# Kernel optimization log

Hardware: AMD Instinct MI355X
Metric: run time of the kernel (lower is better)

Reference implementation:

```python
import math
import jax, jax.numpy as jnp
import numpy as np

NEG_INF_FILL = 1e-09  # faithful to the source: masked positions get +1e-09, not -inf

B, H, S, D = 2, 16, 2048, 64


def setup_inputs() -> dict:
    key = jax.random.key(0)
    kq, kk, kv = jax.random.split(key, 3)
    q = jax.random.normal(kq, (B, H, S, D), dtype=jnp.float32)
    k = jax.random.normal(kk, (B, H, S, D), dtype=jnp.float32)
    v = jax.random.normal(kv, (B, H, S, D), dtype=jnp.float32)
    # causal boolean mask, broadcast over heads: [B, 1, S, S]
    causal = jnp.tril(jnp.ones((S, S), dtype=bool))
    attention_mask = jnp.broadcast_to(causal[None, None, :, :], (B, 1, S, S))
    return {"q": q, "k": k, "v": v, "attention_mask": attention_mask}


def reference(q, k, v, attention_mask):
    d_k = q.shape[-1]
    # scores: [B, H, S, S]
    scores = jnp.einsum("bhqd,bhkd->bhqk", q, k) / math.sqrt(d_k)
    scores = jnp.where(attention_mask, scores, NEG_INF_FILL)
    attn = jax.nn.softmax(scores, axis=-1)
    # output: [B, H, S, D]
    return jnp.einsum("bhqk,bhkd->bhqd", attn, v)
```

## Files before the change

kernel.cpp:

```cpp
#include <hip/hip_runtime.h>


#define SEQ 2048
#define DIM 64
#define NKT 32
#define KS_STRIDE 72
#define PS_STRIDE 72
#define QSCALE 0.18033688011112042f

typedef _Float16 half_t;
typedef _Float16 half8  __attribute__((ext_vector_type(8)));
typedef _Float16 half4v __attribute__((ext_vector_type(4)));
typedef _Float16 half2v __attribute__((ext_vector_type(2)));
typedef float    float4v __attribute__((ext_vector_type(4)));

#define KIMG_HALFS ((size_t)4194304)
#define WS_NEED    ((size_t)16777216)

__global__ __launch_bounds__(256)
void prep_kernel(const float* __restrict__ K, const float* __restrict__ V,
                 half_t* __restrict__ Kimg, half_t* __restrict__ VTimg) {
    __shared__ __align__(16) half_t vt[64 * 72];
    const int kt = blockIdx.x, bh = blockIdx.y;
    const int tid = threadIdx.x;
    const float* Kt = K + ((size_t)bh * SEQ + kt * 64) * DIM;
    const float* Vt = V + ((size_t)bh * SEQ + kt * 64) * DIM;
    half_t* Kd = Kimg  + (((size_t)(bh * NKT + kt)) << 12);
    half_t* Vd = VTimg + (((size_t)(bh * NKT + kt)) << 12);

    {
        const int row = tid >> 2, q = tid & 3;
        const float* src = Kt + row * DIM + 16 * q;
        #pragma unroll
        for (int cc = 0; cc < 2; ++cc) {
            float4v a = *(const float4v*)(src + 8 * cc);
            float4v b = *(const float4v*)(src + 8 * cc + 4);
            half8 hh;
            hh[0]=(half_t)a[0]; hh[1]=(half_t)a[1]; hh[2]=(half_t)a[2]; hh[3]=(half_t)a[3];
            hh[4]=(half_t)b[0]; hh[5]=(half_t)b[1]; hh[6]=(half_t)b[2]; hh[7]=(half_t)b[3];
            *(half8*)(Kd + row * 64 + 16 * q + 8 * cc) = hh;
        }
    }
    {
        const int c = tid & 15, r0 = tid >> 4;
        #pragma unroll
        for (int u = 0; u < 2; ++u) {
            const float* vp = Vt + (size_t)(2 * (r0 + 16 * u)) * DIM + 4 * c;
            float4v x0 = *(const float4v*)(vp);
            float4v x1 = *(const float4v*)(vp + DIM);
            #pragma unroll
            for (int i = 0; i < 4; ++i) {
                const int d = 4 * c + i;
                vt[d * 72 + 2 * (r0 + 16 * u)]     = (half_t)x0[i];
                vt[d * 72 + 2 * (r0 + 16 * u) + 1] = (half_t)x1[i];
            }
        }
    }
    __syncthreads();
    {
        const int d = tid >> 2, g = tid & 3;
        #pragma unroll
        for (int cc = 0; cc < 2; ++cc) {
            const int c0 = 2 * g + cc;
            half8 hh = *(const half8*)(vt + d * 72 + 8 * c0);
            *(half8*)(Vd + d * 64 + 8 * c0) = hh;
        }
    }
}

__global__ __launch_bounds__(256, 4)
void attn_mfma_kernel(const float* __restrict__ Q,
                      const half_t* __restrict__ Kimg,
                      const half_t* __restrict__ VTimg,
                      const float* __restrict__ V,
                      float* __restrict__ O) {
    __shared__ __align__(16) half_t smem_h[64 * KS_STRIDE + 64 * KS_STRIDE + 4 * 16 * PS_STRIDE];
    half_t* Ks  = smem_h;
    half_t* VTs = smem_h + 64 * KS_STRIDE;
    half_t* Ps  = smem_h + 2 * 64 * KS_STRIDE;

    const int tid = threadIdx.x;
    const int l   = tid & 63;
    const int w   = tid >> 6;
    const int lx  = l & 15;
    const int h   = l >> 4;
    const int bh  = blockIdx.x;
    const int qb  = 31 - (int)blockIdx.y;
    const int qbase = qb * 64;
    const int nkt = qb + 1;
    const int n_tail = SEQ - nkt * 64;

    const float* Qh = Q + (size_t)bh * SEQ * DIM;
    const float* Vh = V + (size_t)bh * SEQ * DIM;
    float*       Oh = O + (size_t)bh * SEQ * DIM;
    const half_t* Kimg_b = Kimg  + (((size_t)(bh * NKT)) << 12);
    const half_t* Vimg_b = VTimg + (((size_t)(bh * NKT)) << 12);

    half8 qf[2];
    const int qrow_w = qbase + 16 * w;
    {
        const float* qp = Qh + (size_t)(qrow_w + lx) * DIM;
        #pragma unroll
        for (int s = 0; s < 2; ++s) {
            float4v a = *(const float4v*)(qp + 32 * s + 8 * h);
            float4v b = *(const float4v*)(qp + 32 * s + 8 * h + 4);
            half8 f;
            f[0] = (half_t)(a[0] * QSCALE); f[1] = (half_t)(a[1] * QSCALE);
            f[2] = (half_t)(a[2] * QSCALE); f[3] = (half_t)(a[3] * QSCALE);
            f[4] = (half_t)(b[0] * QSCALE); f[5] = (half_t)(b[1] * QSCALE);
            f[6] = (half_t)(b[2] * QSCALE); f[7] = (half_t)(b[3] * QSCALE);
            qf[s] = f;
        }
    }

    float4v acc[4];
    #pragma unroll
    for (int mt = 0; mt < 4; ++mt) acc[mt] = (float4v){0.f, 0.f, 0.f, 0.f};
    float lp = 0.f;

    const int soff = tid << 3;
    const int srow = tid >> 3;
    const int sc8  = (tid & 7) << 3;
    half8 kh0, kh1, vh0, vh1;
    auto load_tile = [&](int kt) {
        const half_t* Kt16 = Kimg_b + ((size_t)kt << 12);
        const half_t* Vt16 = Vimg_b + ((size_t)kt << 12);
        kh0 = *(const half8*)(Kt16 + soff);
        kh1 = *(const half8*)(Kt16 + soff + 2048);
        vh0 = *(const half8*)(Vt16 + soff);
        vh1 = *(const half8*)(Vt16 + soff + 2048);
    };

    load_tile(0);

    for (int kt = 0; kt < nkt; ++kt) {
        __syncthreads();

        *(half8*)(Ks  + srow * KS_STRIDE + sc8)        = kh0;
        *(half8*)(Ks  + (srow + 32) * KS_STRIDE + sc8) = kh1;
        *(half8*)(VTs + srow * KS_STRIDE + sc8)        = vh0;
        *(half8*)(VTs + (srow + 32) * KS_STRIDE + sc8) = vh1;
        __syncthreads();

        if (kt + 1 < nkt) load_tile(kt + 1);

        const int key_base = kt * 64;
        #pragma unroll
        for (int mt = 0; mt < 4; ++mt) {
            half8 ak0 = *(const half8*)(Ks + (16 * mt + lx) * KS_STRIDE + 8 * h);
            half8 ak1 = *(const half8*)(Ks + (16 * mt + lx) * KS_STRIDE + 32 + 8 * h);
            const bool need_mask = (key_base + 16 * mt + 15) > qrow_w;
            float4v ct = (float4v){0.f, 0.f, 0.f, 0.f};
            ct = __builtin_amdgcn_mfma_f32_16x16x32_f16(ak0, qf[0], ct, 0, 0, 0);
            ct = __builtin_amdgcn_mfma_f32_16x16x32_f16(ak1, qf[1], ct, 0, 0, 0);
            float p[4];
            #pragma unroll
            for (int r = 0; r < 4; ++r)
                p[r] = __builtin_amdgcn_exp2f(ct[r]);
            if (need_mask) {
                const int qg = qrow_w + lx;
                const int kb = key_base + 16 * mt + 4 * h;
                #pragma unroll
                for (int r = 0; r < 4; ++r)
                    if (kb + r > qg) p[r] = 1.0f;
            }
            lp += (p[0] + p[1]) + (p[2] + p[3]);
            half4v hp;
            hp[0] = (half_t)p[0]; hp[1] = (half_t)p[1];
            hp[2] = (half_t)p[2]; hp[3] = (half_t)p[3];
            *(half4v*)(Ps + w * (16 * PS_STRIDE) + lx * PS_STRIDE + 16 * mt + 4 * h) = hp;
        }

        half8 pf[2];
        #pragma unroll
        for (int s = 0; s < 2; ++s)
            pf[s] = *(const half8*)(Ps + w * (16 * PS_STRIDE) + lx * PS_STRIDE
                                    + 32 * s + 8 * h);
        #pragma unroll
        for (int mtd = 0; mtd < 4; ++mtd) {
            half8 av0 = *(const half8*)(VTs + (16 * mtd + lx) * KS_STRIDE + 8 * h);
            half8 av1 = *(const half8*)(VTs + (16 * mtd + lx) * KS_STRIDE + 32 + 8 * h);
            float4v ct = acc[mtd];
            ct = __builtin_amdgcn_mfma_f32_16x16x32_f16(av0, pf[0], ct, 0, 0, 0);
            ct = __builtin_amdgcn_mfma_f32_16x16x32_f16(av1, pf[1], ct, 0, 0, 0);
            acc[mtd] = ct;
        }
    }

    float s_l = lp;
    s_l += __shfl_xor(s_l, 16, 64);
    s_l += __shfl_xor(s_l, 32, 64);
    const float linv = 1.0f / (s_l + (float)n_tail);

    float ts0 = 0.f, ts1 = 0.f, ts2 = 0.f, ts3 = 0.f;
    {
        const int c = tid & 15, r0 = tid >> 4;
        const int tstart = nkt * 64;
        #pragma unroll 4
        for (int k = tstart + r0; k < SEQ; k += 16) {
            float4v x = *(const float4v*)(Vh + (size_t)k * DIM + 4 * c);
            ts0 += x[0]; ts1 += x[1]; ts2 += x[2]; ts3 += x[3];
        }
    }
    __syncthreads();
    float* preS = (float*)smem_h;
    float* vtf  = ((float*)smem_h) + 4160;
    {
        const int c = tid & 15, r0 = tid >> 4;
        float4v pv = {ts0, ts1, ts2, ts3};
        *(float4v*)(preS + r0 * 68 + 4 * c) = pv;
    }
    __syncthreads();
    if (tid < 64) {
        float s = 0.f;
        #pragma unroll
        for (int p = 0; p < 16; ++p) s += preS[p * 68 + tid];
        vtf[tid] = s;
    }
    __syncthreads();
    float vt_l[4][4];
    #pragma unroll
    for (int mt = 0; mt < 4; ++mt)
        #pragma unroll
        for (int r = 0; r < 4; ++r) vt_l[mt][r] = vtf[16 * mt + 4 * h + r];

    float* Osm = (float*)smem_h;
    #pragma unroll
    for (int mt = 0; mt < 4; ++mt)
        #pragma unroll
        for (int r = 0; r < 4; ++r) {
            float o = (acc[mt][r] + vt_l[mt][r]) * linv;
            Osm[w * (16 * 65) + lx * 65 + 16 * mt + 4 * h + r] = o;
        }
    __syncthreads();
    {
        const int c = tid & 15, r0 = tid >> 4;
        #pragma unroll
        for (int u = 0; u < 4; ++u) {
            const int row = r0 + 16 * u;
            const int dc = 4 * c;
            const float* src = Osm + (row >> 4) * (16 * 65) + (row & 15) * 65 + dc;
            float4v ov = {src[0], src[1], src[2], src[3]};
            *(float4v*)(Oh + (size_t)(qbase + row) * DIM + dc) = ov;
        }
    }
}

__global__ __launch_bounds__(256, 4)
void attn_mfma_fallback(const float* __restrict__ Q,
                        const float* __restrict__ K,
                        const float* __restrict__ V,
                        float* __restrict__ O) {
    __shared__ half_t smem_h[64 * KS_STRIDE + 64 * KS_STRIDE + 4 * 16 * PS_STRIDE];
    half_t* Ks  = smem_h;
    half_t* VTs = smem_h + 64 * KS_STRIDE;
    half_t* Ps  = smem_h + 2 * 64 * KS_STRIDE;

    const int tid = threadIdx.x;
    const int l   = tid & 63;
    const int w   = tid >> 6;
    const int lx  = l & 15;
    const int h   = l >> 4;
    const int bh  = blockIdx.x;
    const int qb  = 31 - (int)blockIdx.y;
    const int qbase = qb * 64;
    const int nkt = qb + 1;
    const int n_tail = SEQ - nkt * 64;

    const float* Qh = Q + (size_t)bh * SEQ * DIM;
    const float* Kh = K + (size_t)bh * SEQ * DIM;
    const float* Vh = V + (size_t)bh * SEQ * DIM;
    float*       Oh = O + (size_t)bh * SEQ * DIM;

    half8 qf[2];
    const int qrow_w = qbase + 16 * w;
    {
        const float* qp = Qh + (size_t)(qrow_w + lx) * DIM;
        #pragma unroll
        for (int s = 0; s < 2; ++s) {
            float4v a = *(const float4v*)(qp + 32 * s + 8 * h);
            float4v b = *(const float4v*)(qp + 32 * s + 8 * h + 4);
            half8 f;
            f[0] = (half_t)(a[0] * QSCALE); f[1] = (half_t)(a[1] * QSCALE);
            f[2] = (half_t)(a[2] * QSCALE); f[3] = (half_t)(a[3] * QSCALE);
            f[4] = (half_t)(b[0] * QSCALE); f[5] = (half_t)(b[1] * QSCALE);
            f[6] = (half_t)(b[2] * QSCALE); f[7] = (half_t)(b[3] * QSCALE);
            qf[s] = f;
        }
    }

    float4v acc[4];
    #pragma unroll
    for (int mt = 0; mt < 4; ++mt) acc[mt] = (float4v){0.f, 0.f, 0.f, 0.f};
    float lp = 0.f;

    const int c  = tid & 15;
    const int r0 = tid >> 4;

    float4v kreg[4], vreg[4];
    auto load_tile = [&](int kt) {
        const float* Kt = Kh + (size_t)kt * 64 * DIM;
        const float* Vt = Vh + (size_t)kt * 64 * DIM;
        #pragma unroll
        for (int u = 0; u < 4; ++u)
            kreg[u] = *(const float4v*)(Kt + (r0 + 16 * u) * DIM + 4 * c);
        #pragma unroll
        for (int u = 0; u < 2; ++u) {
            const float* vp = Vt + (size_t)(2 * (r0 + 16 * u)) * DIM + 4 * c;
            vreg[2 * u]     = *(const float4v*)(vp);
            vreg[2 * u + 1] = *(const float4v*)(vp + DIM);
        }
    };

    load_tile(0);

    for (int kt = 0; kt < nkt; ++kt) {
        __syncthreads();
        #pragma unroll
        for (int u = 0; u < 4; ++u) {
            int kr = r0 + 16 * u;
            half4v hk;
            hk[0] = (half_t)kreg[u][0]; hk[1] = (half_t)kreg[u][1];
            hk[2] = (half_t)kreg[u][2]; hk[3] = (half_t)kreg[u][3];
            *(half4v*)(Ks + kr * KS_STRIDE + 4 * c) = hk;
        }
        #pragma unroll
        for (int u = 0; u < 2; ++u) {
            int kp = r0 + 16 * u;
            #pragma unroll
            for (int i = 0; i < 4; ++i) {
                int ir = (i + c + (c >> 2)) & 3;
                int dr = 4 * c + ir;
                half2v hv;
                hv[0] = (half_t)vreg[2 * u][ir];
                hv[1] = (half_t)vreg[2 * u + 1][ir];
                *(half2v*)(VTs + dr * KS_STRIDE + 2 * kp) = hv;
            }
        }
        __syncthreads();

        if (kt + 1 < nkt) load_tile(kt + 1);

        const int key_base = kt * 64;
        #pragma unroll
        for (int mt = 0; mt < 4; ++mt) {
            half8 ak0 = *(const half8*)(Ks + (16 * mt + lx) * KS_STRIDE + 8 * h);
            half8 ak1 = *(const half8*)(Ks + (16 * mt + lx) * KS_STRIDE + 32 + 8 * h);
            const bool need_mask = (key_base + 16 * mt + 15) > qrow_w;
            float4v ct = (float4v){0.f, 0.f, 0.f, 0.f};
            ct = __builtin_amdgcn_mfma_f32_16x16x32_f16(ak0, qf[0], ct, 0, 0, 0);
            ct = __builtin_amdgcn_mfma_f32_16x16x32_f16(ak1, qf[1], ct, 0, 0, 0);
            float p[4];
            #pragma unroll
            for (int r = 0; r < 4; ++r)
                p[r] = __builtin_amdgcn_exp2f(ct[r]);
            if (need_mask) {
                const int qg = qrow_w + lx;
                const int kb = key_base + 16 * mt + 4 * h;
                #pragma unroll
                for (int r = 0; r < 4; ++r)
                    if (kb + r > qg) p[r] = 1.0f;
            }
            lp += (p[0] + p[1]) + (p[2] + p[3]);
            half4v hp;
            hp[0] = (half_t)p[0]; hp[1] = (half_t)p[1];
            hp[2] = (half_t)p[2]; hp[3] = (half_t)p[3];
            *(half4v*)(Ps + w * (16 * PS_STRIDE) + lx * PS_STRIDE + 16 * mt + 4 * h) = hp;
        }

        half8 pf[2];
        #pragma unroll
        for (int s = 0; s < 2; ++s)
            pf[s] = *(const half8*)(Ps + w * (16 * PS_STRIDE) + lx * PS_STRIDE
                                    + 32 * s + 8 * h);
        #pragma unroll
        for (int mtd = 0; mtd < 4; ++mtd) {
            half8 av0 = *(const half8*)(VTs + (16 * mtd + lx) * KS_STRIDE + 8 * h);
            half8 av1 = *(const half8*)(VTs + (16 * mtd + lx) * KS_STRIDE + 32 + 8 * h);
            float4v ct = acc[mtd];
            ct = __builtin_amdgcn_mfma_f32_16x16x32_f16(av0, pf[0], ct, 0, 0, 0);
            ct = __builtin_amdgcn_mfma_f32_16x16x32_f16(av1, pf[1], ct, 0, 0, 0);
            acc[mtd] = ct;
        }
    }

    float s_l = lp;
    s_l += __shfl_xor(s_l, 16, 64);
    s_l += __shfl_xor(s_l, 32, 64);
    const float linv = 1.0f / (s_l + (float)n_tail);

    float ts0 = 0.f, ts1 = 0.f, ts2 = 0.f, ts3 = 0.f;
    {
        const int tstart = nkt * 64;
        #pragma unroll 4
        for (int k = tstart + r0; k < SEQ; k += 16) {
            float4v x = *(const float4v*)(Vh + (size_t)k * DIM + 4 * c);
            ts0 += x[0]; ts1 += x[1]; ts2 += x[2]; ts3 += x[3];
        }
    }
    __syncthreads();
    float* preS = (float*)smem_h;
    float* vtf  = ((float*)smem_h) + 4160;
    {
        float4v pv = {ts0, ts1, ts2, ts3};
        *(float4v*)(preS + r0 * 68 + 4 * c) = pv;
    }
    __syncthreads();
    if (tid < 64) {
        float s = 0.f;
        #pragma unroll
        for (int p = 0; p < 16; ++p) s += preS[p * 68 + tid];
        vtf[tid] = s;
    }
    __syncthreads();
    float vt_l[4][4];
    #pragma unroll
    for (int mt = 0; mt < 4; ++mt)
        #pragma unroll
        for (int r = 0; r < 4; ++r) vt_l[mt][r] = vtf[16 * mt + 4 * h + r];

    float* Osm = (float*)smem_h;
    #pragma unroll
    for (int mt = 0; mt < 4; ++mt)
        #pragma unroll
        for (int r = 0; r < 4; ++r) {
            float o = (acc[mt][r] + vt_l[mt][r]) * linv;
            Osm[w * (16 * 65) + lx * 65 + 16 * mt + 4 * h + r] = o;
        }
    __syncthreads();
    #pragma unroll
    for (int u = 0; u < 4; ++u) {
        int row = r0 + 16 * u;
        int dc = 4 * c;
        const float* src = Osm + (row >> 4) * (16 * 65) + (row & 15) * 65 + dc;
        float4v ov = {src[0], src[1], src[2], src[3]};
        *(float4v*)(Oh + (size_t)(qbase + row) * DIM + dc) = ov;
    }
}

extern "C" void kernel_launch(void* const* d_in, const int* in_sizes, int n_in,
                              void* d_out, int out_size, void* d_ws, size_t ws_size,
                              hipStream_t stream) {
    const float* q = (const float*)d_in[0];
    const float* k = (const float*)d_in[1];
    const float* v = (const float*)d_in[2];
    float* out = (float*)d_out;

    if (d_ws != nullptr && ws_size >= WS_NEED) {
        half_t* kimg = (half_t*)d_ws;
        half_t* vimg = kimg + KIMG_HALFS;
        prep_kernel<<<dim3(32, 32), 256, 0, stream>>>(k, v, kimg, vimg);
        attn_mfma_kernel<<<dim3(32, 32), 256, 0, stream>>>(q, kimg, vimg, v, out);
    } else {
        attn_mfma_fallback<<<dim3(32, 32), 256, 0, stream>>>(q, k, v, out);
    }
}
```

Baseline: 144.6 us.

## Stage K/V tiles via direct global-to-LDS loads with swizzle and precomputed V suffix sums

The prep kernel now writes K and V-transpose images with an XOR swizzle. The attention kernel streams each 64-key tile straight into double-buffered LDS with global_load_lds, which removes the register round trip and one barrier per iteration. A new suffix_kernel precomputes per-tile suffix sums of V, so each block reads a 64-float row instead of re-reducing the masked tail of V. This adds an extra launch and workspace, and depends on the swizzle matching between writer and reader.

```diff
diff --git a/kernel.cpp b/kernel.cpp
--- a/kernel.cpp
+++ b/kernel.cpp
@@ -4,8 +4,6 @@
 #define SEQ 2048
 #define DIM 64
 #define NKT 32
-#define KS_STRIDE 72
-#define PS_STRIDE 72
 #define QSCALE 0.18033688011112042f
 
 typedef _Float16 half_t;
@@ -15,18 +13,24 @@
 typedef float    float4v __attribute__((ext_vector_type(4)));
 
 #define KIMG_HALFS ((size_t)4194304)
-#define WS_NEED    ((size_t)16777216)
+#define WS_NEED    ((size_t)17039360)
+
+__device__ __forceinline__ void glds16(const void* g, void* l) {
+    __builtin_amdgcn_global_load_lds((const __attribute__((address_space(1))) void*)g,
+                                     (__attribute__((address_space(3))) void*)l,
+                                     16, 0, 0);
+}
 
 __global__ __launch_bounds__(256)
 void prep_kernel(const float* __restrict__ K, const float* __restrict__ V,
-                 half_t* __restrict__ Kimg, half_t* __restrict__ VTimg) {
+                 half_t* __restrict__ Kimg, half_t* __restrict__ Vimg) {
     __shared__ __align__(16) half_t vt[64 * 72];
     const int kt = blockIdx.x, bh = blockIdx.y;
     const int tid = threadIdx.x;
     const float* Kt = K + ((size_t)bh * SEQ + kt * 64) * DIM;
     const float* Vt = V + ((size_t)bh * SEQ + kt * 64) * DIM;
-    half_t* Kd = Kimg  + (((size_t)(bh * NKT + kt)) << 12);
-    half_t* Vd = VTimg + (((size_t)(bh * NKT + kt)) << 12);
+    half_t* Kd = Kimg + (((size_t)(bh * NKT + kt)) << 12);
+    half_t* Vd = Vimg + (((size_t)(bh * NKT + kt)) << 12);
 
     {
         const int row = tid >> 2, q = tid & 3;
@@ -38,7 +42,8 @@
             half8 hh;
             hh[0]=(half_t)a[0]; hh[1]=(half_t)a[1]; hh[2]=(half_t)a[2]; hh[3]=(half_t)a[3];
             hh[4]=(half_t)b[0]; hh[5]=(half_t)b[1]; hh[6]=(half_t)b[2]; hh[7]=(half_t)b[3];
-            *(half8*)(Kd + row * 64 + 16 * q + 8 * cc) = hh;
+            const int sc = (2 * q + cc) ^ (row & 7);
+            *(half8*)(Kd + row * 64 + sc * 8) = hh;
         }
     }
     {
@@ -63,21 +68,36 @@
         for (int cc = 0; cc < 2; ++cc) {
             const int c0 = 2 * g + cc;
             half8 hh = *(const half8*)(vt + d * 72 + 8 * c0);
-            *(half8*)(Vd + d * 64 + 8 * c0) = hh;
-        }
-    }
+            const int sc = c0 ^ (d & 7);
+            *(half8*)(Vd + d * 64 + sc * 8) = hh;
+        }
+    }
+}
+
+__global__ __launch_bounds__(256)
+void suffix_kernel(const float* __restrict__ V, float* __restrict__ Stab) {
+    __shared__ float part[32 * 9];
+    const int dg = blockIdx.x, bh = blockIdx.y;
+    const int t = threadIdx.x >> 3, dl = threadIdx.x & 7;
+    const int d = dg * 8 + dl;
+    const float* Vb = V + (size_t)bh * SEQ * DIM;
+    float s = 0.f;
+    #pragma unroll 8
+    for (int j = 0; j < 64; ++j) s += Vb[(size_t)(t * 64 + j) * DIM + d];
+    part[t * 9 + dl] = s;
+    __syncthreads();
+    float r = 0.f;
+    for (int tt = 31; tt >= t; --tt) r += part[tt * 9 + dl];
+    Stab[((size_t)bh * 32 + t) * 64 + d] = r;
 }
 
 __global__ __launch_bounds__(256, 4)
 void attn_mfma_kernel(const float* __restrict__ Q,
                       const half_t* __restrict__ Kimg,
-                      const half_t* __restrict__ VTimg,
-                      const float* __restrict__ V,
+                      const half_t* __restrict__ Vimg,
+                      const float* __restrict__ Stab,
                       float* __restrict__ O) {
-    __shared__ __align__(16) half_t smem_h[64 * KS_STRIDE + 64 * KS_STRIDE + 4 * 16 * PS_STRIDE];
-    half_t* Ks  = smem_h;
-    half_t* VTs = smem_h + 64 * KS_STRIDE;
-    half_t* Ps  = smem_h + 2 * 64 * KS_STRIDE;
+    __shared__ __align__(16) half_t smem_h[20480];
 
     const int tid = threadIdx.x;
     const int l   = tid & 63;
@@ -91,10 +111,7 @@
     const int n_tail = SEQ - nkt * 64;
 
     const float* Qh = Q + (size_t)bh * SEQ * DIM;
-    const float* Vh = V + (size_t)bh * SEQ * DIM;
     float*       Oh = O + (size_t)bh * SEQ * DIM;
-    const half_t* Kimg_b = Kimg  + (((size_t)(bh * NKT)) << 12);
-    const half_t* Vimg_b = VTimg + (((size_t)(bh * NKT)) << 12);
 
     half8 qf[2];
     const int qrow_w = qbase + 16 * w;
@@ -118,28 +135,213 @@
     for (int mt = 0; mt < 4; ++mt) acc[mt] = (float4v){0.f, 0.f, 0.f, 0.f};
     float lp = 0.f;
 
-    const int soff = tid << 3;
-    const int srow = tid >> 3;
-    const int sc8  = (tid & 7) << 3;
-    half8 kh0, kh1, vh0, vh1;
+    const size_t tile0 = ((size_t)(bh * NKT)) << 13;
+    auto stage = [&](int kt, int buf) {
+        const size_t toff = tile0 + ((size_t)kt << 13);
+        const char* gk = (const char*)Kimg + toff + (tid << 4);
+        const char* gv = (const char*)Vimg + toff + (tid << 4);
+        char* lk = (char*)smem_h + (buf << 13) + (w << 10);
+        char* lv = (char*)smem_h + 16384 + (buf << 13) + (w << 10);
+        glds16(gk, lk);  glds16(gk + 4096, lk + 4096);
+        glds16(gv, lv);  glds16(gv + 4096, lv + 4096);
+    };
+
+    const int sx  = lx & 7;
+    const int o0h = (h ^ sx) << 3;
+    const int o1h = ((h + 4) ^ sx) << 3;
+    half_t* Psw = smem_h + 16384 + (w << 10);
+
+    stage(0, 0);
+    asm volatile("s_waitcnt vmcnt(0)" ::: "memory");
+    __syncthreads();
+
+    int cur = 0;
+    for (int kt = 0; kt < nkt; ++kt) {
+        if (kt + 1 < nkt) stage(kt + 1, cur ^ 1);
+
+        const half_t* Kb = smem_h + cur * 4096 + (lx << 6);
+        const half_t* Vb = smem_h + 8192 + cur * 4096 + (lx << 6);
+        const int key_base = kt << 6;
+
+        #pragma unroll
+        for (int mt = 0; mt < 4; ++mt) {
+            half8 ak0 = *(const half8*)(Kb + (mt << 10) + o0h);
+            half8 ak1 = *(const half8*)(Kb + (mt << 10) + o1h);
+            float4v ct = (float4v){0.f, 0.f, 0.f, 0.f};
+            ct = __builtin_amdgcn_mfma_f32_16x16x32_f16(ak0, qf[0], ct, 0, 0, 0);
+            ct = __builtin_amdgcn_mfma_f32_16x16x32_f16(ak1, qf[1], ct, 0, 0, 0);
+            float p[4];
+            #pragma unroll
+            for (int r = 0; r < 4; ++r)
+                p[r] = __builtin_amdgcn_exp2f(ct[r]);
+            if ((key_base + 16 * mt + 15) > qrow_w) {
+                const int qg = qrow_w + lx;
+                const int kb = key_base + 16 * mt + 4 * h;
+                #pragma unroll
+                for (int r = 0; r < 4; ++r)
+                    if (kb + r > qg) p[r] = 1.0f;
+            }
+            lp += (p[0] + p[1]) + (p[2] + p[3]);
+            half4v hp;
+            hp[0] = (half_t)p[0]; hp[1] = (half_t)p[1];
+            hp[2] = (half_t)p[2]; hp[3] = (half_t)p[3];
+            *(half4v*)(Psw + (lx << 6)
+                       + ((((mt << 1) + (h >> 1)) ^ sx) << 3) + ((h & 1) << 2)) = hp;
+        }
+
+        half8 pf0 = *(const half8*)(Psw + (lx << 6) + o0h);
+        half8 pf1 = *(const half8*)(Psw + (lx << 6) + o1h);
+        #pragma unroll
+        for (int mtd = 0; mtd < 4; ++mtd) {
+            half8 av0 = *(const half8*)(Vb + (mtd << 10) + o0h);
+            half8 av1 = *(const half8*)(Vb + (mtd << 10) + o1h);
+            float4v ct = acc[mtd];
+            ct = __builtin_amdgcn_mfma_f32_16x16x32_f16(av0, pf0, ct, 0, 0, 0);
+            ct = __builtin_amdgcn_mfma_f32_16x16x32_f16(av1, pf1, ct, 0, 0, 0);
+            acc[mtd] = ct;
+        }
+
+        asm volatile("s_waitcnt vmcnt(0)" ::: "memory");
+        __syncthreads();
+        cur ^= 1;
+    }
+
+    float s_l = lp;
+    s_l += __shfl_xor(s_l, 16, 64);
+    s_l += __shfl_xor(s_l, 32, 64);
+    const float linv = 1.0f / (s_l + (float)n_tail);
+
+    float vt_l[4][4];
+    if (n_tail > 0) {
+        const float* Sr = Stab + (((size_t)bh << 5) + nkt) * 64;
+        #pragma unroll
+        for (int mt = 0; mt < 4; ++mt) {
+            float4v x = *(const float4v*)(Sr + 16 * mt + 4 * h);
+            vt_l[mt][0] = x[0]; vt_l[mt][1] = x[1];
+            vt_l[mt][2] = x[2]; vt_l[mt][3] = x[3];
+        }
+    } else {
+        #pragma unroll
+        for (int mt = 0; mt < 4; ++mt)
+            vt_l[mt][0] = vt_l[mt][1] = vt_l[mt][2] = vt_l[mt][3] = 0.f;
+    }
+
+    float* Osm = (float*)smem_h;
+    #pragma unroll
+    for (int mt = 0; mt < 4; ++mt)
+        #pragma unroll
+        for (int r = 0; r < 4; ++r) {
+            float o = (acc[mt][r] + vt_l[mt][r]) * linv;
+            Osm[w * (16 * 65) + lx * 65 + 16 * mt + 4 * h + r] = o;
+        }
+    __syncthreads();
+    {
+        const int c = tid & 15, r0 = tid >> 4;
+        #pragma unroll
+        for (int u = 0; u < 4; ++u) {
+            const int row = r0 + 16 * u;
+            const int dc = 4 * c;
+            const float* src = Osm + (row >> 4) * (16 * 65) + (row & 15) * 65 + dc;
+            float4v ov = {src[0], src[1], src[2], src[3]};
+            *(float4v*)(Oh + (size_t)(qbase + row) * DIM + dc) = ov;
+        }
+    }
+}
+
+#define KS_STRIDE 72
+#define PS_STRIDE 72
+
+__global__ __launch_bounds__(256, 4)
+void attn_mfma_fallback(const float* __restrict__ Q,
+                        const float* __restrict__ K,
+                        const float* __restrict__ V,
+                        float* __restrict__ O) {
+    __shared__ half_t smem_h[64 * KS_STRIDE + 64 * KS_STRIDE + 4 * 16 * PS_STRIDE];
+    half_t* Ks  = smem_h;
+    half_t* VTs = smem_h + 64 * KS_STRIDE;
+    half_t* Ps  = smem_h + 2 * 64 * KS_STRIDE;
+
+    const int tid = threadIdx.x;
+    const int l   = tid & 63;
+    const int w   = tid >> 6;
+    const int lx  = l & 15;
+    const int h   = l >> 4;
+    const int bh  = blockIdx.x;
+    const int qb  = 31 - (int)blockIdx.y;
+    const int qbase = qb * 64;
+    const int nkt = qb + 1;
+    const int n_tail = SEQ - nkt * 64;
+
+    const float* Qh = Q + (size_t)bh * SEQ * DIM;
+    const float* Kh = K + (size_t)bh * SEQ * DIM;
+    const float* Vh = V + (size_t)bh * SEQ * DIM;
+    float*       Oh = O + (size_t)bh * SEQ * DIM;
+
+    half8 qf[2];
+    const int qrow_w = qbase + 16 * w;
+    {
+        const float* qp = Qh + (size_t)(qrow_w + lx) * DIM;
+        #pragma unroll
+        for (int s = 0; s < 2; ++s) {
+            float4v a = *(const float4v*)(qp + 32 * s + 8 * h);
+            float4v b = *(const float4v*)(qp + 32 * s + 8 * h + 4);
+            half8 f;
+            f[0] = (half_t)(a[0] * QSCALE); f[1] = (half_t)(a[1] * QSCALE);
+            f[2] = (half_t)(a[2] * QSCALE); f[3] = (half_t)(a[3] * QSCALE);
+            f[4] = (half_t)(b[0] * QSCALE); f[5] = (half_t)(b[1] * QSCALE);
+            f[6] = (half_t)(b[2] * QSCALE); f[7] = (half_t)(b[3] * QSCALE);
+            qf[s] = f;
+        }
+    }
+
+    float4v acc[4];
+    #pragma unroll
+    for (int mt = 0; mt < 4; ++mt) acc[mt] = (float4v){0.f, 0.f, 0.f, 0.f};
+    float lp = 0.f;
+
+    const int c  = tid & 15;
+    const int r0 = tid >> 4;
+
+    float4v kreg[4], vreg[4];
     auto load_tile = [&](int kt) {
-        const half_t* Kt16 = Kimg_b + ((size_t)kt << 12);
-        const half_t* Vt16 = Vimg_b + ((size_t)kt << 12);
-        kh0 = *(const half8*)(Kt16 + soff);
-        kh1 = *(const half8*)(Kt16 + soff + 2048);
-        vh0 = *(const half8*)(Vt16 + soff);
-        vh1 = *(const half8*)(Vt16 + soff + 2048);
+        const float* Kt = Kh + (size_t)kt * 64 * DIM;
+        const float* Vt = Vh + (size_t)kt * 64 * DIM;
+        #pragma unroll
+        for (int u = 0; u < 4; ++u)
+            kreg[u] = *(const float4v*)(Kt + (r0 + 16 * u) * DIM + 4 * c);
+        #pragma unroll
+        for (int u = 0; u < 2; ++u) {
+            const float* vp = Vt + (size_t)(2 * (r0 + 16 * u)) * DIM + 4 * c;
+            vreg[2 * u]     = *(const float4v*)(vp);
+            vreg[2 * u + 1] = *(const float4v*)(vp + DIM);
+        }
     };
 
     load_tile(0);
 
     for (int kt = 0; kt < nkt; ++kt) {
         __syncthreads();
-
-        *(half8*)(Ks  + srow * KS_STRIDE + sc8)        = kh0;
-        *(half8*)(Ks  + (srow + 32) * KS_STRIDE + sc8) = kh1;
-        *(half8*)(VTs + srow * KS_STRIDE + sc8)        = vh0;
-        *(half8*)(VTs + (srow + 32) * KS_STRIDE + sc8) = vh1;
+        #pragma unroll
+        for (int u = 0; u < 4; ++u) {
+            int kr = r0 + 16 * u;
+            half4v hk;
+            hk[0] = (half_t)kreg[u][0]; hk[1] = (half_t)kreg[u][1];
+            hk[2] = (half_t)kreg[u][2]; hk[3] = (half_t)kreg[u][3];
+            *(half4v*)(Ks + kr * KS_STRIDE + 4 * c) = hk;
+        }
+        #pragma unroll
+        for (int u = 0; u < 2; ++u) {
+            int kp = r0 + 16 * u;
+            #pragma unroll
+            for (int i = 0; i < 4; ++i) {
+                int ir = (i + c + (c >> 2)) & 3;
+                int dr = 4 * c + ir;
+                half2v hv;
+                hv[0] = (half_t)vreg[2 * u][ir];
+                hv[1] = (half_t)vreg[2 * u + 1][ir];
+                *(half2v*)(VTs + dr * KS_STRIDE + 2 * kp) = hv;
+            }
+        }
         __syncthreads();
 
         if (kt + 1 < nkt) load_tile(kt + 1);
@@ -194,203 +396,6 @@
 
     float ts0 = 0.f, ts1 = 0.f, ts2 = 0.f, ts3 = 0.f;
     {
-        const int c = tid & 15, r0 = tid >> 4;
-        const int tstart = nkt * 64;
-        #pragma unroll 4
-        for (int k = tstart + r0; k < SEQ; k += 16) {
-            float4v x = *(const float4v*)(Vh + (size_t)k * DIM + 4 * c);
-            ts0 += x[0]; ts1 += x[1]; ts2 += x[2]; ts3 += x[3];
-        }
-    }
-    __syncthreads();
-    float* preS = (float*)smem_h;
-    float* vtf  = ((float*)smem_h) + 4160;
-    {
-        const int c = tid & 15, r0 = tid >> 4;
-        float4v pv = {ts0, ts1, ts2, ts3};
-        *(float4v*)(preS + r0 * 68 + 4 * c) = pv;
-    }
-    __syncthreads();
-    if (tid < 64) {
-        float s = 0.f;
-        #pragma unroll
-        for (int p = 0; p < 16; ++p) s += preS[p * 68 + tid];
-        vtf[tid] = s;
-    }
-    __syncthreads();
-    float vt_l[4][4];
-    #pragma unroll
-    for (int mt = 0; mt < 4; ++mt)
-        #pragma unroll
-        for (int r = 0; r < 4; ++r) vt_l[mt][r] = vtf[16 * mt + 4 * h + r];
-
-    float* Osm = (float*)smem_h;
-    #pragma unroll
-    for (int mt = 0; mt < 4; ++mt)
-        #pragma unroll
-        for (int r = 0; r < 4; ++r) {
-            float o = (acc[mt][r] + vt_l[mt][r]) * linv;
-            Osm[w * (16 * 65) + lx * 65 + 16 * mt + 4 * h + r] = o;
-        }
-    __syncthreads();
-    {
-        const int c = tid & 15, r0 = tid >> 4;
-        #pragma unroll
-        for (int u = 0; u < 4; ++u) {
-            const int row = r0 + 16 * u;
-            const int dc = 4 * c;
-            const float* src = Osm + (row >> 4) * (16 * 65) + (row & 15) * 65 + dc;
-            float4v ov = {src[0], src[1], src[2], src[3]};
-            *(float4v*)(Oh + (size_t)(qbase + row) * DIM + dc) = ov;
-        }
-    }
-}
-
-__global__ __launch_bounds__(256, 4)
-void attn_mfma_fallback(const float* __restrict__ Q,
-                        const float* __restrict__ K,
-                        const float* __restrict__ V,
-                        float* __restrict__ O) {
-    __shared__ half_t smem_h[64 * KS_STRIDE + 64 * KS_STRIDE + 4 * 16 * PS_STRIDE];
-    half_t* Ks  = smem_h;
-    half_t* VTs = smem_h + 64 * KS_STRIDE;
-    half_t* Ps  = smem_h + 2 * 64 * KS_STRIDE;
-
-    const int tid = threadIdx.x;
-    const int l   = tid & 63;
-    const int w   = tid >> 6;
-    const int lx  = l & 15;
-    const int h   = l >> 4;
-    const int bh  = blockIdx.x;
-    const int qb  = 31 - (int)blockIdx.y;
-    const int qbase = qb * 64;
-    const int nkt = qb + 1;
-    const int n_tail = SEQ - nkt * 64;
-
-    const float* Qh = Q + (size_t)bh * SEQ * DIM;
-    const float* Kh = K + (size_t)bh * SEQ * DIM;
-    const float* Vh = V + (size_t)bh * SEQ * DIM;
-    float*       Oh = O + (size_t)bh * SEQ * DIM;
-
-    half8 qf[2];
-    const int qrow_w = qbase + 16 * w;
-    {
-        const float* qp = Qh + (size_t)(qrow_w + lx) * DIM;
-        #pragma unroll
-        for (int s = 0; s < 2; ++s) {
-            float4v a = *(const float4v*)(qp + 32 * s + 8 * h);
-            float4v b = *(const float4v*)(qp + 32 * s + 8 * h + 4);
-            half8 f;
-            f[0] = (half_t)(a[0] * QSCALE); f[1] = (half_t)(a[1] * QSCALE);
-            f[2] = (half_t)(a[2] * QSCALE); f[3] = (half_t)(a[3] * QSCALE);
-            f[4] = (half_t)(b[0] * QSCALE); f[5] = (half_t)(b[1] * QSCALE);
-            f[6] = (half_t)(b[2] * QSCALE); f[7] = (half_t)(b[3] * QSCALE);
-            qf[s] = f;
-        }
-    }
-
-    float4v acc[4];
-    #pragma unroll
-    for (int mt = 0; mt < 4; ++mt) acc[mt] = (float4v){0.f, 0.f, 0.f, 0.f};
-    float lp = 0.f;
-
-    const int c  = tid & 15;
-    const int r0 = tid >> 4;
-
-    float4v kreg[4], vreg[4];
-    auto load_tile = [&](int kt) {
-        const float* Kt = Kh + (size_t)kt * 64 * DIM;
-        const float* Vt = Vh + (size_t)kt * 64 * DIM;
-        #pragma unroll
-        for (int u = 0; u < 4; ++u)
-            kreg[u] = *(const float4v*)(Kt + (r0 + 16 * u) * DIM + 4 * c);
-        #pragma unroll
-        for (int u = 0; u < 2; ++u) {
-            const float* vp = Vt + (size_t)(2 * (r0 + 16 * u)) * DIM + 4 * c;
-            vreg[2 * u]     = *(const float4v*)(vp);
-            vreg[2 * u + 1] = *(const float4v*)(vp + DIM);
-        }
-    };
-
-    load_tile(0);
-
-    for (int kt = 0; kt < nkt; ++kt) {
-        __syncthreads();
-        #pragma unroll
-        for (int u = 0; u < 4; ++u) {
-            int kr = r0 + 16 * u;
-            half4v hk;
-            hk[0] = (half_t)kreg[u][0]; hk[1] = (half_t)kreg[u][1];
-            hk[2] = (half_t)kreg[u][2]; hk[3] = (half_t)kreg[u][3];
-            *(half4v*)(Ks + kr * KS_STRIDE + 4 * c) = hk;
-        }
-        #pragma unroll
-        for (int u = 0; u < 2; ++u) {
-            int kp = r0 + 16 * u;
-            #pragma unroll
-            for (int i = 0; i < 4; ++i) {
-                int ir = (i + c + (c >> 2)) & 3;
-                int dr = 4 * c + ir;
-                half2v hv;
-                hv[0] = (half_t)vreg[2 * u][ir];
-                hv[1] = (half_t)vreg[2 * u + 1][ir];
-                *(half2v*)(VTs + dr * KS_STRIDE + 2 * kp) = hv;
-            }
-        }
-        __syncthreads();
-
-        if (kt + 1 < nkt) load_tile(kt + 1);
-
-        const int key_base = kt * 64;
-        #pragma unroll
-        for (int mt = 0; mt < 4; ++mt) {
-            half8 ak0 = *(const half8*)(Ks + (16 * mt + lx) * KS_STRIDE + 8 * h);
-            half8 ak1 = *(const half8*)(Ks + (16 * mt + lx) * KS_STRIDE + 32 + 8 * h);
-            const bool need_mask = (key_base + 16 * mt + 15) > qrow_w;
-            float4v ct = (float4v){0.f, 0.f, 0.f, 0.f};
-            ct = __builtin_amdgcn_mfma_f32_16x16x32_f16(ak0, qf[0], ct, 0, 0, 0);
-            ct = __builtin_amdgcn_mfma_f32_16x16x32_f16(ak1, qf[1], ct, 0, 0, 0);
-            float p[4];
-            #pragma unroll
-            for (int r = 0; r < 4; ++r)
-                p[r] = __builtin_amdgcn_exp2f(ct[r]);
-            if (need_mask) {
-                const int qg = qrow_w + lx;
-                const int kb = key_base + 16 * mt + 4 * h;
-                #pragma unroll
-                for (int r = 0; r < 4; ++r)
-                    if (kb + r > qg) p[r] = 1.0f;
-            }
-            lp += (p[0] + p[1]) + (p[2] + p[3]);
-            half4v hp;
-            hp[0] = (half_t)p[0]; hp[1] = (half_t)p[1];
-            hp[2] = (half_t)p[2]; hp[3] = (half_t)p[3];
-            *(half4v*)(Ps + w * (16 * PS_STRIDE) + lx * PS_STRIDE + 16 * mt + 4 * h) = hp;
-        }
-
-        half8 pf[2];
-        #pragma unroll
-        for (int s = 0; s < 2; ++s)
-            pf[s] = *(const half8*)(Ps + w * (16 * PS_STRIDE) + lx * PS_STRIDE
-                                    + 32 * s + 8 * h);
-        #pragma unroll
-        for (int mtd = 0; mtd < 4; ++mtd) {
-            half8 av0 = *(const half8*)(VTs + (16 * mtd + lx) * KS_STRIDE + 8 * h);
-            half8 av1 = *(const half8*)(VTs + (16 * mtd + lx) * KS_STRIDE + 32 + 8 * h);
-            float4v ct = acc[mtd];
-            ct = __builtin_amdgcn_mfma_f32_16x16x32_f16(av0, pf[0], ct, 0, 0, 0);
-            ct = __builtin_amdgcn_mfma_f32_16x16x32_f16(av1, pf[1], ct, 0, 0, 0);
-            acc[mtd] = ct;
-        }
-    }
-
-    float s_l = lp;
-    s_l += __shfl_xor(s_l, 16, 64);
-    s_l += __shfl_xor(s_l, 32, 64);
-    const float linv = 1.0f / (s_l + (float)n_tail);
-
-    float ts0 = 0.f, ts1 = 0.f, ts2 = 0.f, ts3 = 0.f;
-    {
         const int tstart = nkt * 64;
         #pragma unroll 4
         for (int k = tstart + r0; k < SEQ; k += 16) {
@@ -449,8 +454,10 @@
     if (d_ws != nullptr && ws_size >= WS_NEED) {
         half_t* kimg = (half_t*)d_ws;
         half_t* vimg = kimg + KIMG_HALFS;
+        float*  stab = (float*)((char*)d_ws + 16777216);
         prep_kernel<<<dim3(32, 32), 256, 0, stream>>>(k, v, kimg, vimg);
-        attn_mfma_kernel<<<dim3(32, 32), 256, 0, stream>>>(q, kimg, vimg, v, out);
+        suffix_kernel<<<dim3(8, 32), 256, 0, stream>>>(v, stab);
+        attn_mfma_kernel<<<dim3(32, 32), 256, 0, stream>>>(q, kimg, vimg, stab, out);
     } else {
         attn_mfma_fallback<<<dim3(32, 32), 256, 0, stream>>>(q, k, v, out);
     }
```

New measurement: 150.0 us. +3.7%, slower.
